# Performance work log

Hardware: AMD Instinct MI355X
Metric: run time of the kernel (lower is better)

Reference implementation:

```python
import jax, jax.numpy as jnp
import numpy as np

BLOCK_SIZE = 8
SELECT_TOPK = 32
HIDDEN = 512
CHANNELS = 384
NUM_HEADS = 8
B, H, W = 8, 64, 64


def setup_inputs() -> dict:
    key = jax.random.key(0)
    ks = jax.random.split(key, 8)
    num_block_tot = (H // BLOCK_SIZE) * (W // BLOCK_SIZE)
    bs2 = BLOCK_SIZE * BLOCK_SIZE
    x = jax.random.normal(ks[0], (B, H, W, CHANNELS), dtype=jnp.float32)
    aw = jax.random.normal(ks[1], (NUM_HEADS, B, num_block_tot, bs2, bs2 + SELECT_TOPK), dtype=jnp.float32)
    attn_weights = jax.nn.softmax(aw, axis=-1)  # module expects sum(-1)==1
    weights = jax.random.uniform(ks[2], (B, num_block_tot, SELECT_TOPK), dtype=jnp.float32)
    indexes = jax.random.randint(ks[3], (B, num_block_tot, SELECT_TOPK), 0, H * W)
    in_proj_w = jax.random.normal(ks[4], (3 * HIDDEN, CHANNELS), dtype=jnp.float32) * 0.02
    in_proj_b = jax.random.normal(ks[5], (3 * HIDDEN,), dtype=jnp.float32) * 0.02
    out_proj_w = jax.random.normal(ks[6], (CHANNELS, HIDDEN), dtype=jnp.float32) * 0.02
    out_proj_b = jax.random.normal(ks[7], (CHANNELS,), dtype=jnp.float32) * 0.02
    return {"x": x, "attn_weights": attn_weights, "weights": weights,
            "in_proj_w": in_proj_w, "in_proj_b": in_proj_b,
            "out_proj_w": out_proj_w, "out_proj_b": out_proj_b,
            "indexes": indexes}


def reference(x, attn_weights, weights, in_proj_w, in_proj_b, out_proj_w, out_proj_b, indexes):
    batch, height, width, _ = x.shape
    bsz = BLOCK_SIZE
    nbh, nbw = height // bsz, width // bsz
    nbt = nbh * nbw
    num_heads = attn_weights.shape[0]
    hid = HIDDEN
    hd = hid // num_heads
    topk = SELECT_TOPK

    proj = jnp.einsum('bhwc,oc->bhwo', x, in_proj_w) + in_proj_b  # (B,H,W,3*hid)
    s, xh, y = jnp.split(proj, 3, axis=-1)
    xh = xh * jnp.tanh(s)  # Balancer/Whiten/Identity are identity in fwd

    # top-k gathered tokens: (B, nbt, topk, hid) without (B,nbt,num_tokens,hid) blowup
    x_flat = xh.reshape(batch, height * width, hid)
    sel = jax.vmap(lambda xf, ix: xf[ix])(x_flat, indexes)  # (B,nbt,topk,hid)
    sel = sel * weights[..., None]
    sel = sel.reshape(batch, nbt, topk, num_heads, hd).transpose(3, 0, 1, 2, 4)  # (nh,B,nbt,topk,hd)

    # block-local tokens: (nh, B, nbt, bsz^2, hd)
    blk = xh.reshape(batch, nbh, bsz, nbw, bsz, num_heads, hd)
    blk = blk.transpose(5, 0, 1, 3, 2, 4, 6).reshape(num_heads, batch, nbt, bsz * bsz, hd)

    kv = jnp.concatenate([blk, sel], axis=3)  # (nh,B,nbt,bsz^2+topk,hd)
    out = jnp.einsum('hbnqk,hbnkd->hbnqd', attn_weights, kv)  # (nh,B,nbt,bsz^2,hd)

    out = out.reshape(num_heads, batch, nbh, nbw, bsz, bsz, hd)
    out = out.transpose(1, 2, 4, 3, 5, 0, 6).reshape(batch, height, width, hid)
    out = out * y
    return jnp.einsum('bhwd,cd->bhwc', out, out_proj_w) + out_proj_b
```

## Files before the change

### kernel.cpp

```cpp
#include <hip/hip_runtime.h>
#include <hip/hip_bf16.h>
#include <stdint.h>

#define CH   384
#define HID  512
#define NHD  8
#define MTOT 32768

typedef __attribute__((ext_vector_type(8))) short bf16x8;
typedef __attribute__((ext_vector_type(4))) float f32x4;
typedef unsigned short u16;

__device__ __forceinline__ float bf2f(u16 v){ return __uint_as_float(((unsigned)v)<<16); }
__device__ __forceinline__ u16 f2bf(float f){
  unsigned u = __float_as_uint(f);
  return (u16)((u + 0x7fffu + ((u>>16)&1u)) >> 16);
}
__device__ __forceinline__ float fast_tanh(float s){
  float e = __expf(2.f*s);
  return 1.f - 2.f*__builtin_amdgcn_rcpf(e + 1.f);
}
__device__ __forceinline__ void gload_lds16(const void* g, void* l){
  __builtin_amdgcn_global_load_lds((const __attribute__((address_space(1))) void*)g,
                                   (__attribute__((address_space(3))) void*)l, 16, 0, 0);
}

#define CVT_N1 (MTOT*CH/4)
#define CVT_N2 (3*HID*CH/4)
#define CVT_N3 (CH*HID/4)
__global__ void k_cvt3(const float* __restrict__ x,  u16* __restrict__ xo,
                       const float* __restrict__ w1, u16* __restrict__ w1o,
                       const float* __restrict__ w2, u16* __restrict__ w2o){
  const int total = CVT_N1 + CVT_N2 + CVT_N3;
  int i = blockIdx.x*blockDim.x + threadIdx.x;
  int stride = gridDim.x*blockDim.x;
  for (; i < total; i += stride){
    const float4* src; ushort4* dst; int k;
    if (i < CVT_N1){ src = (const float4*)x;  dst = (ushort4*)xo;  k = i; }
    else if (i < CVT_N1 + CVT_N2){ src = (const float4*)w1; dst = (ushort4*)w1o; k = i - CVT_N1; }
    else { src = (const float4*)w2; dst = (ushort4*)w2o; k = i - CVT_N1 - CVT_N2; }
    float4 v = src[k];
    ushort4 o; o.x=f2bf(v.x); o.y=f2bf(v.y); o.z=f2bf(v.z); o.w=f2bf(v.w);
    dst[k] = o;
  }
}

__global__ __launch_bounds__(256)
void k_gemm1(const u16* __restrict__ xb, const u16* __restrict__ w1b,
             const float* __restrict__ b1,
             u16* __restrict__ xh, u16* __restrict__ yb)
{
  __shared__ short lds[14336];
  const int tid = threadIdx.x;
  const int w = tid >> 6, lw = tid & 63;
  const int bid = blockIdx.x;
  const int xcd = bid & 7, ii = bid >> 3;
  const int m0 = (xcd*32 + (ii >> 4)) * 128;
  const int h0 = (ii & 15) * 32;
  const int lc = lw & 15, lk = lw >> 4;

  f32x4 acc[2][6] = {};

  const int sl = (lw & 7) ^ (lw >> 3);
  const int rsub = lw >> 3;
  const u16* gsrc[7]; int ldst[7];
  #pragma unroll
  for (int i = 0; i < 7; ++i){
    int c = w*7 + i;
    if (c < 16){
      int r = c*8 + rsub;
      gsrc[i] = xb + (size_t)(m0 + r)*CH + sl*8;
      ldst[i] = c*512;
    } else {
      int rb = (c-16)*8 + rsub;
      int grow = (rb >> 5)*HID + h0 + (rb & 31);
      gsrc[i] = w1b + (size_t)grow*CH + sl*8;
      ldst[i] = 8192 + (c-16)*512;
    }
  }

  #pragma unroll 1
  for (int kt = 0; kt < 6; ++kt){
    #pragma unroll
    for (int i = 0; i < 7; ++i)
      gload_lds16(gsrc[i] + kt*64, &lds[ldst[i]]);
    __syncthreads();
    #pragma unroll
    for (int ks = 0; ks < 2; ++ks){
      const int s = (ks*4 + lk) ^ (lc & 7);
      bf16x8 af[2], bfr[6];
      #pragma unroll
      for (int mi = 0; mi < 2; ++mi){
        int row = w*32 + mi*16 + lc;
        af[mi] = *(const bf16x8*)&lds[row*64 + s*8];
      }
      #pragma unroll
      for (int nj = 0; nj < 6; ++nj){
        int row = nj*16 + lc;
        bfr[nj] = *(const bf16x8*)&lds[8192 + row*64 + s*8];
      }
      #pragma unroll
      for (int mi = 0; mi < 2; ++mi)
        #pragma unroll
        for (int nj = 0; nj < 6; ++nj)
          acc[mi][nj] = __builtin_amdgcn_mfma_f32_16x16x32_bf16(af[mi], bfr[nj], acc[mi][nj], 0,0,0);
    }
    __syncthreads();
  }

  {
    short* epx = &lds[w*2560];
    short* epy = &lds[w*2560 + 1280];
    float bs[2], bx[2], by[2];
    #pragma unroll
    for (int f = 0; f < 2; ++f){
      int col = h0 + f*16 + lc;
      bs[f] = b1[col]; bx[f] = b1[512 + col]; by[f] = b1[1024 + col];
    }
    #pragma unroll
    for (int mi = 0; mi < 2; ++mi)
      #pragma unroll
      for (int f = 0; f < 2; ++f)
        #pragma unroll
        for (int j = 0; j < 4; ++j){
          float sv = acc[mi][0+f][j] + bs[f];
          float xv = (acc[mi][2+f][j] + bx[f]) * fast_tanh(sv);
          float yv = acc[mi][4+f][j] + by[f];
          int row = mi*16 + lk*4 + j;
          epx[row*40 + f*16 + lc] = (short)f2bf(xv);
          epy[row*40 + f*16 + lc] = (short)f2bf(yv);
        }
    __syncthreads();
    const int row = lw >> 1, half = lw & 1;
    const size_t gbase = (size_t)(m0 + w*32 + row)*HID + h0 + half*16;
    #pragma unroll
    for (int q = 0; q < 2; ++q){
      bf16x8 v = *(const bf16x8*)&epx[row*40 + half*16 + q*8];
      *(bf16x8*)&xh[gbase + q*8] = v;
    }
    #pragma unroll
    for (int q = 0; q < 2; ++q){
      bf16x8 v = *(const bf16x8*)&epy[row*40 + half*16 + q*8];
      *(bf16x8*)&yb[gbase + q*8] = v;
    }
  }
}

__global__ __launch_bounds__(64, 3)
void k_attn(const float* __restrict__ aw, const float* __restrict__ wts,
            const int* __restrict__ idxs,
            const u16* __restrict__ xh, const u16* __restrict__ yb,
            u16* __restrict__ zb)
{
  __shared__ short lKv[64*96];
  const int tid = threadIdx.x;
  const int bid = blockIdx.x;
  const int h = bid >> 9;
  const int b = (bid >> 6) & 7;
  const int n = bid & 63;
  const int bh = n >> 3, bw = n & 7;

  {
    const int dg = tid & 7;
    const int pr = tid >> 3;
    #pragma unroll
    for (int it = 0; it < 6; ++it){
      int pair = it*8 + pr;
      int t0 = pair*2;
      size_t r0, r1;
      if (t0 < 64){
        int pix = (bh*8 + (t0>>3))*64 + bw*8 + (t0&7);
        r0 = (size_t)b*4096 + pix;
        r1 = r0 + 1;
      } else {
        int e = (b*64+n)*32 + (t0-64);
        r0 = (size_t)b*4096 + idxs[e];
        r1 = (size_t)b*4096 + idxs[e+1];
      }
      bf16x8 v0 = *(const bf16x8*)&xh[r0*HID + h*64 + dg*8];
      bf16x8 v1 = *(const bf16x8*)&xh[r1*HID + h*64 + dg*8];
      #pragma unroll
      for (int j = 0; j < 8; ++j){
        int d = dg*8 + j;
        int elem = (d*96 + t0) ^ (dg<<3);
        unsigned pk = (unsigned)(u16)v0[j] | ((unsigned)(u16)v1[j] << 16);
        *(unsigned*)&lKv[elem] = pk;
      }
    }
  }
  __syncthreads();

  float wv[8];
  {
    const float* wp = wts + (size_t)(b*64+n)*32 + (tid>>4)*8;
    float4 a = *(const float4*)wp, c = *(const float4*)(wp+4);
    wv[0]=a.x; wv[1]=a.y; wv[2]=a.z; wv[3]=a.w;
    wv[4]=c.x; wv[5]=c.y; wv[6]=c.z; wv[7]=c.w;
  }
  const float* awp = aw + (size_t)bid * (64*96);
  bf16x8 af[3][4];
  #pragma unroll
  for (int ks = 0; ks < 3; ++ks){
    #pragma unroll
    for (int mi = 0; mi < 4; ++mi){
      const float* p = awp + (size_t)(mi*16 + (tid&15))*96 + ks*32 + (tid>>4)*8;
      float4 f0 = *(const float4*)p;
      float4 f1 = *(const float4*)(p+4);
      float t[8] = {f0.x,f0.y,f0.z,f0.w,f1.x,f1.y,f1.z,f1.w};
      #pragma unroll
      for (int j = 0; j < 8; ++j){
        float v = (ks == 2) ? t[j]*wv[j] : t[j];
        af[ks][mi][j] = (short)f2bf(v);
      }
    }
  }

  bf16x8 yv[8];
  {
    int pix = (bh*8 + (tid>>3))*64 + bw*8 + (tid&7);
    const u16* yrow = yb + ((size_t)b*4096 + pix)*HID + h*64;
    #pragma unroll
    for (int c = 0; c < 8; ++c)
      yv[c] = *(const bf16x8*)&yrow[c*8];
  }

  f32x4 acc[4][4] = {};
  const int lc = tid & 15, lk = tid >> 4;
  #pragma unroll
  for (int ks = 0; ks < 3; ++ks){
    bf16x8 bv[4];
    #pragma unroll
    for (int nj = 0; nj < 4; ++nj){
      int d = nj*16 + lc;
      int idx = (d*96 + ks*32 + lk*8) ^ ((d>>3)<<3);
      bv[nj] = *(const bf16x8*)&lKv[idx];
    }
    #pragma unroll
    for (int mi = 0; mi < 4; ++mi)
      #pragma unroll
      for (int nj = 0; nj < 4; ++nj)
        acc[mi][nj] = __builtin_amdgcn_mfma_f32_16x16x32_bf16(af[ks][mi], bv[nj], acc[mi][nj], 0,0,0);
  }

  {
    const int q = tid;
    #pragma unroll
    for (int c = 0; c < 8; ++c)
      *(bf16x8*)&lKv[q*72 + c*8] = yv[c];
  }

  #pragma unroll
  for (int mi = 0; mi < 4; ++mi){
    #pragma unroll
    for (int nj = 0; nj < 4; ++nj){
      int d = nj*16 + lc;
      size_t gcol = (size_t)h*64 + d;
      #pragma unroll
      for (int j = 0; j < 4; ++j){
        int q = mi*16 + lk*4 + j;
        int pix = (bh*8 + (q>>3))*64 + bw*8 + (q&7);
        size_t r = (size_t)b*4096 + pix;
        float yvf = bf2f((u16)lKv[q*72 + d]);
        zb[r*HID + gcol] = f2bf(acc[mi][nj][j] * yvf);
      }
    }
  }
}

__global__ __launch_bounds__(256)
void k_gemm2(const u16* __restrict__ zb, const u16* __restrict__ w2b,
             const float* __restrict__ b2, float* __restrict__ out)
{
  __shared__ short lds[16384];
  const int tid = threadIdx.x;
  const int w = tid>>6, lw = tid&63;
  const int wm = w>>1, wn = w&1;
  const int bid = blockIdx.x;
  const int xcd = bid & 7, ii = bid >> 3;
  const int m0 = (xcd*32 + ii/3) * 128;
  const int n0 = (ii%3) * 128;
  const int lc = lw & 15, lk = lw >> 4;

  f32x4 acc[4][4] = {};

  const int sl_g = (lw & 3) ^ ((lw >> 3) & 3);
  const int rsub = lw >> 2;
  const u16* gsrc[4]; int ldst[4];
  #pragma unroll
  for (int i = 0; i < 4; ++i){
    int c = w*4 + i;
    if (c < 8){
      int r = c*16 + rsub;
      gsrc[i] = zb + (size_t)(m0+r)*HID + sl_g*8;
      ldst[i] = c*512;
    } else {
      int cb = c - 8;
      int r = cb*16 + rsub;
      gsrc[i] = w2b + (size_t)(n0+r)*HID + sl_g*8;
      ldst[i] = 4096 + cb*512;
    }
  }
  auto STAGE = [&](int buf, int kt){
    #pragma unroll
    for (int i = 0; i < 4; ++i)
      gload_lds16(gsrc[i] + kt*32, &lds[ldst[i] + buf*8192]);
  };
  const int skey = (lc >> 1) & 3;
  auto COMPUTE = [&](int buf){
    const short* pa = lds + buf*8192;
    const short* pb = lds + buf*8192 + 4096;
    bf16x8 af[4], bb[4];
    #pragma unroll
    for (int mi=0; mi<4; ++mi){
      int row = wm*64 + mi*16 + lc;
      af[mi] = *(const bf16x8*)&pa[row*32 + (lk ^ skey)*8];
    }
    #pragma unroll
    for (int nj=0; nj<4; ++nj){
      int row = wn*64 + nj*16 + lc;
      bb[nj] = *(const bf16x8*)&pb[row*32 + (lk ^ skey)*8];
    }
    #pragma unroll
    for (int mi=0; mi<4; ++mi)
      #pragma unroll
      for (int nj=0; nj<4; ++nj)
        acc[mi][nj] = __builtin_amdgcn_mfma_f32_16x16x32_bf16(af[mi], bb[nj], acc[mi][nj], 0,0,0);
  };

  STAGE(0, 0);
  #pragma unroll 1
  for (int kt = 0; kt < 16; ++kt){
    if (kt < 15){
      STAGE((kt+1)&1, kt+1);
      asm volatile("s_waitcnt vmcnt(4)" ::: "memory");
    } else {
      asm volatile("s_waitcnt vmcnt(0)" ::: "memory");
    }
    __builtin_amdgcn_sched_barrier(0);
    __builtin_amdgcn_s_barrier();
    COMPUTE(kt&1);
    __builtin_amdgcn_sched_barrier(0);
    __builtin_amdgcn_s_barrier();
  }

  const int lr4 = lk*4;
  #pragma unroll
  for (int nj=0; nj<4; ++nj){
    int col = n0 + wn*64 + nj*16 + lc;
    float bias = b2[col];
    #pragma unroll
    for (int mi=0; mi<4; ++mi){
      #pragma unroll
      for (int j=0; j<4; ++j){
        int row = m0 + wm*64 + mi*16 + lr4 + j;
        out[(size_t)row*CH + col] = acc[mi][nj][j] + bias;
      }
    }
  }
}

extern "C" void kernel_launch(void* const* d_in, const int* in_sizes, int n_in,
                              void* d_out, int out_size, void* d_ws, size_t ws_size,
                              hipStream_t stream) {
  const float* x   = (const float*)d_in[0];
  const float* aw  = (const float*)d_in[1];
  const float* wts = (const float*)d_in[2];
  const float* w1  = (const float*)d_in[3];
  const float* b1  = (const float*)d_in[4];
  const float* w2  = (const float*)d_in[5];
  const float* b2  = (const float*)d_in[6];
  const int*   idx = (const int*)d_in[7];
  float* out = (float*)d_out;

  char* ws = (char*)d_ws;
  u16* x_bf  = (u16*)(ws);
  u16* w1_bf = (u16*)(ws + 25165824);
  u16* w2_bf = (u16*)(ws + 26345472);
  u16* xh_bf = (u16*)(ws + 26738688);
  u16* y_bf  = (u16*)(ws + 60293120);
  u16* z_bf  = (u16*)(ws + 93847552);

  k_cvt3<<<2048, 256, 0, stream>>>(x, x_bf, w1, w1_bf, w2, w2_bf);

  k_gemm1<<<4096, 256, 0, stream>>>(x_bf, w1_bf, b1, xh_bf, y_bf);
  k_attn<<<NHD*8*64, 64, 0, stream>>>(aw, wts, idx, xh_bf, y_bf, z_bf);
  k_gemm2<<<768, 256, 0, stream>>>(z_bf, w2_bf, b2, out);
}
```

Before: 145.8 us.

## Prepack attention weights to bf16 MFMA layout inside gemm1, add packed attn kernel

The fp32 attention weights are converted to bf16 inside gemm1, with the top-k selection weights folded into the last 32 columns. They are written in the exact per-lane MFMA fragment order. A new attention kernel then loads the fragments directly as bf16x8 vectors instead of reading and converting fp32 and scaling gathered rows. This is meant to shrink the attention kernel's heavy fp32 traffic and per-element work. The cost is an extra full fp32 read plus bf16 write of the weights in gemm1, and an extra 50MB of workspace, with a fallback to the old kernel when the workspace is too small.

```diff
diff --git a/kernel.cpp b/kernel.cpp
--- a/kernel.cpp
+++ b/kernel.cpp
@@ -48,7 +48,9 @@
 __global__ __launch_bounds__(256)
 void k_gemm1(const u16* __restrict__ xb, const u16* __restrict__ w1b,
              const float* __restrict__ b1,
-             u16* __restrict__ xh, u16* __restrict__ yb)
+             u16* __restrict__ xh, u16* __restrict__ yb,
+             const float* __restrict__ awf, const float* __restrict__ wts,
+             u16* __restrict__ awb)
 {
   __shared__ short lds[14336];
   const int tid = threadIdx.x;
@@ -106,6 +108,32 @@
           acc[mi][nj] = __builtin_amdgcn_mfma_f32_16x16x32_bf16(af[mi], bfr[nj], acc[mi][nj], 0,0,0);
     }
     __syncthreads();
+  }
+
+  if (awb){
+    const int tile = bid;
+    const float* awt = awf + (size_t)tile*6144;
+    u16* awo = awb + (size_t)tile*6144;
+    #pragma unroll
+    for (int rep = 0; rep < 3; ++rep){
+      int c = tid + rep*256;
+      int mi = (c >> 6) & 3;
+      int lane = c & 63;
+      const float* p = awt + (mi*16 + (lane&15))*96 + rep*32 + (lane>>4)*8;
+      float4 f0 = *(const float4*)p, f1 = *(const float4*)(p+4);
+      float t[8] = {f0.x,f0.y,f0.z,f0.w,f1.x,f1.y,f1.z,f1.w};
+      if (rep == 2){
+        const float* wp = wts + (size_t)(tile & 511)*32 + (lane>>4)*8;
+        float4 a = *(const float4*)wp, cc = *(const float4*)(wp+4);
+        float wv8[8] = {a.x,a.y,a.z,a.w,cc.x,cc.y,cc.z,cc.w};
+        #pragma unroll
+        for (int j = 0; j < 8; ++j) t[j] *= wv8[j];
+      }
+      bf16x8 o;
+      #pragma unroll
+      for (int j = 0; j < 8; ++j) o[j] = (short)f2bf(t[j]);
+      *(bf16x8*)&awo[c*8] = o;
+    }
   }
 
   {
@@ -147,6 +175,111 @@
 }
 
 __global__ __launch_bounds__(64, 3)
+void k_attn_pk(const u16* __restrict__ awb, const int* __restrict__ idxs,
+               const u16* __restrict__ xh, const u16* __restrict__ yb,
+               u16* __restrict__ zb)
+{
+  __shared__ short lKv[64*96];
+  const int tid = threadIdx.x;
+  const int bid = blockIdx.x;
+  const int h = bid >> 9;
+  const int b = (bid >> 6) & 7;
+  const int n = bid & 63;
+  const int bh = n >> 3, bw = n & 7;
+
+  {
+    const int dg = tid & 7;
+    const int pr = tid >> 3;
+    #pragma unroll
+    for (int it = 0; it < 6; ++it){
+      int pair = it*8 + pr;
+      int t0 = pair*2;
+      size_t r0, r1;
+      if (t0 < 64){
+        int pix = (bh*8 + (t0>>3))*64 + bw*8 + (t0&7);
+        r0 = (size_t)b*4096 + pix;
+        r1 = r0 + 1;
+      } else {
+        int e = (b*64+n)*32 + (t0-64);
+        r0 = (size_t)b*4096 + idxs[e];
+        r1 = (size_t)b*4096 + idxs[e+1];
+      }
+      bf16x8 v0 = *(const bf16x8*)&xh[r0*HID + h*64 + dg*8];
+      bf16x8 v1 = *(const bf16x8*)&xh[r1*HID + h*64 + dg*8];
+      #pragma unroll
+      for (int j = 0; j < 8; ++j){
+        int d = dg*8 + j;
+        int elem = (d*96 + t0) ^ (dg<<3);
+        unsigned pk = (unsigned)(u16)v0[j] | ((unsigned)(u16)v1[j] << 16);
+        *(unsigned*)&lKv[elem] = pk;
+      }
+    }
+  }
+  __syncthreads();
+
+  bf16x8 af[3][4];
+  {
+    const u16* awp = awb + (size_t)bid*6144 + tid*8;
+    #pragma unroll
+    for (int ks = 0; ks < 3; ++ks)
+      #pragma unroll
+      for (int mi = 0; mi < 4; ++mi)
+        af[ks][mi] = *(const bf16x8*)&awp[(ks*256 + mi*64)*8];
+  }
+
+  bf16x8 yv[8];
+  {
+    int pix = (bh*8 + (tid>>3))*64 + bw*8 + (tid&7);
+    const u16* yrow = yb + ((size_t)b*4096 + pix)*HID + h*64;
+    #pragma unroll
+    for (int c = 0; c < 8; ++c)
+      yv[c] = *(const bf16x8*)&yrow[c*8];
+  }
+
+  f32x4 acc[4][4] = {};
+  const int lc = tid & 15, lk = tid >> 4;
+  #pragma unroll
+  for (int ks = 0; ks < 3; ++ks){
+    bf16x8 bv[4];
+    #pragma unroll
+    for (int nj = 0; nj < 4; ++nj){
+      int d = nj*16 + lc;
+      int idx = (d*96 + ks*32 + lk*8) ^ ((d>>3)<<3);
+      bv[nj] = *(const bf16x8*)&lKv[idx];
+    }
+    #pragma unroll
+    for (int mi = 0; mi < 4; ++mi)
+      #pragma unroll
+      for (int nj = 0; nj < 4; ++nj)
+        acc[mi][nj] = __builtin_amdgcn_mfma_f32_16x16x32_bf16(af[ks][mi], bv[nj], acc[mi][nj], 0,0,0);
+  }
+
+  {
+    const int q = tid;
+    #pragma unroll
+    for (int c = 0; c < 8; ++c)
+      *(bf16x8*)&lKv[q*72 + c*8] = yv[c];
+  }
+
+  #pragma unroll
+  for (int mi = 0; mi < 4; ++mi){
+    #pragma unroll
+    for (int nj = 0; nj < 4; ++nj){
+      int d = nj*16 + lc;
+      size_t gcol = (size_t)h*64 + d;
+      #pragma unroll
+      for (int j = 0; j < 4; ++j){
+        int q = mi*16 + lk*4 + j;
+        int pix = (bh*8 + (q>>3))*64 + bw*8 + (q&7);
+        size_t r = (size_t)b*4096 + pix;
+        float yvf = bf2f((u16)lKv[q*72 + d]);
+        zb[r*HID + gcol] = f2bf(acc[mi][nj][j] * yvf);
+      }
+    }
+  }
+}
+
+__global__ __launch_bounds__(64, 3)
 void k_attn(const float* __restrict__ aw, const float* __restrict__ wts,
             const int* __restrict__ idxs,
             const u16* __restrict__ xh, const u16* __restrict__ yb,
@@ -379,10 +512,15 @@
   u16* xh_bf = (u16*)(ws + 26738688);
   u16* y_bf  = (u16*)(ws + 60293120);
   u16* z_bf  = (u16*)(ws + 93847552);
+  const size_t need = 127401984ull + 50331648ull;
+  u16* aw_bf = (ws_size >= need) ? (u16*)(ws + 127401984) : (u16*)nullptr;
 
   k_cvt3<<<2048, 256, 0, stream>>>(x, x_bf, w1, w1_bf, w2, w2_bf);
 
-  k_gemm1<<<4096, 256, 0, stream>>>(x_bf, w1_bf, b1, xh_bf, y_bf);
-  k_attn<<<NHD*8*64, 64, 0, stream>>>(aw, wts, idx, xh_bf, y_bf, z_bf);
+  k_gemm1<<<4096, 256, 0, stream>>>(x_bf, w1_bf, b1, xh_bf, y_bf, aw, wts, aw_bf);
+  if (aw_bf)
+    k_attn_pk<<<NHD*8*64, 64, 0, stream>>>(aw_bf, idx, xh_bf, y_bf, z_bf);
+  else
+    k_attn<<<NHD*8*64, 64, 0, stream>>>(aw, wts, idx, xh_bf, y_bf, z_bf);
   k_gemm2<<<768, 256, 0, stream>>>(z_bf, w2_bf, b2, out);
 }
```

Result: slower. 151.9 us (+4.2%).
